# Kernel optimization log

Hardware: AMD Instinct MI355X
Metric: run time of the kernel (lower is better)

## Reference

```python
import jax, jax.numpy as jnp
import numpy as np

B, C, H, W = 16, 64, 224, 224
KS, STRIDE, PAD = 3, 2, 1
S = KS * KS           # patch_size = 9
G = C                 # group=1 -> inc//group = 64 independent ScannCore heads
P_SIDE = (H + 2 * PAD - KS) // STRIDE + 1   # 112
P = P_SIDE * P_SIDE                          # 12544 patches


def _unfold(x):
    """F.unfold(x, KS, 1, PAD, STRIDE) -> [B, C, S, Ph, Pw], (kh, kw) ordering."""
    xp = jnp.pad(x, ((0, 0), (0, 0), (PAD, PAD), (PAD, PAD)))
    end = 1 + STRIDE * (P_SIDE - 1)
    pats = [xp[:, :, kh:kh + end:STRIDE, kw:kw + end:STRIDE]
            for kh in range(KS) for kw in range(KS)]
    return jnp.stack(pats, axis=2)  # [B, C, S, Ph, Pw]


def setup_inputs() -> dict:
    key = jax.random.key(0)
    ks = jax.random.split(key, 10)
    x = jax.random.normal(ks[0], (B, C, H, W), dtype=jnp.float32)
    lim = 1.0 / np.sqrt(S)
    u = lambda k, shape: jax.random.uniform(k, shape, jnp.float32, -lim, lim)
    return {
        "x": x,
        "Wq": u(ks[1], (G, S, S)), "bq": u(ks[2], (G, S)),
        "Wk": u(ks[3], (G, S, S)), "bk": u(ks[4], (G, S)),
        "Wv": u(ks[5], (G, S, S)), "bv": u(ks[6], (G, S)),
        "Wo": u(ks[7], (G, 1, S)), "bo": u(ks[8], (G, 1)),
    }


def reference(x, Wq, bq, Wk, bk, Wv, bv, Wo, bo):
    # unfold -> [B, G, P, S] (group=1, so each channel is its own group)
    t = _unfold(x).reshape(B, G, S, P).transpose(0, 1, 3, 2)
    # per-group linear projections (torch Linear: y = x @ W.T + b)
    Q = jnp.einsum('bgps,gts->bgpt', t, Wq) + bq[None, :, None, :]
    K = jnp.einsum('bgps,gts->bgpt', t, Wk) + bk[None, :, None, :]
    V = jnp.einsum('bgps,gts->bgpt', t, Wv) + bv[None, :, None, :]
    # energy = K^T @ Q over the patch axis -> [B, G, S, S]
    energy = jnp.einsum('bgps,bgpt->bgst', K, Q)
    att = jax.nn.softmax(energy, axis=-1)
    # y = (att @ V^T)^T -> [B, G, P, S]
    y = jnp.einsum('bgst,bgpt->bgps', att, V)
    # out Linear(S -> 1), then fold back to [B, C, side, side]
    out = jnp.einsum('bgps,gos->bgpo', y, Wo) + bo[None, :, None, :]  # [B,G,P,1]
    return out[..., 0].reshape(B, G, P_SIDE, P_SIDE)
```

## Files before the change

kernel.cpp:

```cpp
#include <hip/hip_runtime.h>

#define HH 224
#define WW 224
#define PSD 112
#define NP 12544
#define NBG 1024
#define NCH 28
#define NTASK (112 * NCH)

#define MIDX(i, j) (9 * (i) - (i) * ((i)-1) / 2 + ((j) - (i)))
#define MAT(i, j) ((i) <= (j) ? sh[MIDX(i, j)] : sh[MIDX(j, i)])

__device__ __forceinline__ void load_row9(const float* __restrict__ row,
                                          int t, float* L) {
    const int cb = 8 * t;
    L[0] = (t == 0) ? 0.f : row[cb - 1];
    float4 a = *reinterpret_cast<const float4*>(row + cb);
    float4 b = *reinterpret_cast<const float4*>(row + cb + 4);
    L[1] = a.x; L[2] = a.y; L[3] = a.z; L[4] = a.w;
    L[5] = b.x; L[6] = b.y; L[7] = b.z; L[8] = b.w;
}

__global__ __launch_bounds__(256, 4) void scann_k(
    const float* __restrict__ x,
    const float* __restrict__ Wq, const float* __restrict__ bq,
    const float* __restrict__ Wk, const float* __restrict__ bk,
    const float* __restrict__ Wv, const float* __restrict__ bv,
    const float* __restrict__ Wo, const float* __restrict__ bo,
    float* __restrict__ out) {
    const int bg = blockIdx.x;
    const int g = bg & 63;
    const float* __restrict__ xp = x + (size_t)bg * (HH * WW);
    const int tid = threadIdx.x;

    __shared__ float red[4][56];
    __shared__ float sh[54];
    __shared__ float TT[81];
    __shared__ float Qm_s[9];
    __shared__ float wsh[81];
    __shared__ float cf[10];

    float acc[45];
    float sm[9];
#pragma unroll
    for (int k = 0; k < 45; ++k) acc[k] = 0.f;
#pragma unroll
    for (int i = 0; i < 9; ++i) sm[i] = 0.f;

    for (int task = tid; task < NTASK; task += 256) {
        const int ph = task / NCH;
        const int t = task - ph * NCH;
        const int r0 = 2 * ph - 1;
        float L[3][9];
#pragma unroll
        for (int kr = 0; kr < 3; ++kr) {
            const int r = r0 + kr;
            if (r < 0) {
#pragma unroll
                for (int j = 0; j < 9; ++j) L[kr][j] = 0.f;
            } else {
                load_row9(xp + r * WW, t, L[kr]);
            }
        }
#pragma unroll
        for (int u = 0; u < 4; ++u) {
            float v[9];
#pragma unroll
            for (int kh = 0; kh < 3; ++kh)
#pragma unroll
                for (int kw = 0; kw < 3; ++kw) v[3 * kh + kw] = L[kh][2 * u + kw];
            int k = 0;
#pragma unroll
            for (int i = 0; i < 9; ++i) {
                sm[i] += v[i];
#pragma unroll
                for (int j = i; j < 9; ++j) {
                    acc[k] += v[i] * v[j];
                    ++k;
                }
            }
        }
    }

    {
        const int lane = tid & 63;
        const int wv = tid >> 6;
#pragma unroll
        for (int k = 0; k < 45; ++k) {
            float v = acc[k];
#pragma unroll
            for (int off = 32; off; off >>= 1) v += __shfl_down(v, off, 64);
            if (lane == 0) red[wv][k] = v;
        }
#pragma unroll
        for (int i = 0; i < 9; ++i) {
            float v = sm[i];
#pragma unroll
            for (int off = 32; off; off >>= 1) v += __shfl_down(v, off, 64);
            if (lane == 0) red[wv][45 + i] = v;
        }
    }
    __syncthreads();
    if (tid < 54)
        sh[tid] = red[0][tid] + red[1][tid] + red[2][tid] + red[3][tid];
    __syncthreads();

    if (tid < 9) {
        const int t = tid;
        const float* wqt = Wq + g * 81 + t * 9;
        float w[9];
#pragma unroll
        for (int j = 0; j < 9; ++j) w[j] = wqt[j];
        float q = 0.f;
#pragma unroll
        for (int j = 0; j < 9; ++j) q += w[j] * sh[45 + j];
        Qm_s[t] = q;
#pragma unroll
        for (int i = 0; i < 9; ++i) {
            float s = 0.f;
#pragma unroll
            for (int j = 0; j < 9; ++j) s += MAT(i, j) * w[j];
            TT[i * 9 + t] = s;
        }
    }
    __syncthreads();
    if (tid < 9) {
        const int s = tid;
        const float* wks = Wk + g * 81 + s * 9;
        float w[9];
#pragma unroll
        for (int i = 0; i < 9; ++i) w[i] = wks[i];
        float Km = 0.f;
#pragma unroll
        for (int i = 0; i < 9; ++i) Km += w[i] * sh[45 + i];
        const float bks = bk[g * 9 + s];
        float e[9];
#pragma unroll
        for (int t = 0; t < 9; ++t) {
            const float bqt = bq[g * 9 + t];
            float sum = bks * Qm_s[t] + bqt * Km + 12544.f * bks * bqt;
#pragma unroll
            for (int i = 0; i < 9; ++i) sum += w[i] * TT[i * 9 + t];
            e[t] = sum;
        }
        float mx = e[0];
#pragma unroll
        for (int t = 1; t < 9; ++t) mx = fmaxf(mx, e[t]);
        float ex[9], se = 0.f;
#pragma unroll
        for (int t = 0; t < 9; ++t) {
            ex[t] = expf(e[t] - mx);
            se += ex[t];
        }
        const float wos = Wo[g * 9 + s] / se;
#pragma unroll
        for (int t = 0; t < 9; ++t) wsh[s * 9 + t] = wos * ex[t];
    }
    __syncthreads();
    if (tid < 9) {
        const int j = tid;
        float weff[9];
#pragma unroll
        for (int t = 0; t < 9; ++t) {
            float s = 0.f;
#pragma unroll
            for (int s2 = 0; s2 < 9; ++s2) s += wsh[s2 * 9 + t];
            weff[t] = s;
        }
        float cj = 0.f;
#pragma unroll
        for (int t = 0; t < 9; ++t) cj += weff[t] * Wv[g * 81 + t * 9 + j];
        cf[j] = cj;
        if (j == 0) {
            float d = bo[g];
#pragma unroll
            for (int t = 0; t < 9; ++t) d += weff[t] * bv[g * 9 + t];
            cf[9] = d;
        }
    }
    __syncthreads();

    float cc[9];
#pragma unroll
    for (int j = 0; j < 9; ++j) cc[j] = cf[j];
    const float dd = cf[9];
    float* __restrict__ op = out + (size_t)bg * NP;

    for (int task = tid; task < NTASK; task += 256) {
        const int ph = task / NCH;
        const int t = task - ph * NCH;
        const int r0 = 2 * ph - 1;
        float L[3][9];
#pragma unroll
        for (int kr = 0; kr < 3; ++kr) {
            const int r = r0 + kr;
            if (r < 0) {
#pragma unroll
                for (int j = 0; j < 9; ++j) L[kr][j] = 0.f;
            } else {
                load_row9(xp + r * WW, t, L[kr]);
            }
        }
        float o[4];
#pragma unroll
        for (int u = 0; u < 4; ++u) {
            float s = dd;
#pragma unroll
            for (int kh = 0; kh < 3; ++kh)
#pragma unroll
                for (int kw = 0; kw < 3; ++kw)
                    s += cc[3 * kh + kw] * L[kh][2 * u + kw];
            o[u] = s;
        }
        *reinterpret_cast<float4*>(op + ph * PSD + 4 * t) =
            make_float4(o[0], o[1], o[2], o[3]);
    }
}

extern "C" void kernel_launch(void* const* d_in, const int* in_sizes, int n_in,
                              void* d_out, int out_size, void* d_ws, size_t ws_size,
                              hipStream_t stream) {
    const float* x = (const float*)d_in[0];
    const float* Wq = (const float*)d_in[1];
    const float* bq = (const float*)d_in[2];
    const float* Wk = (const float*)d_in[3];
    const float* bk = (const float*)d_in[4];
    const float* Wv = (const float*)d_in[5];
    const float* bv = (const float*)d_in[6];
    const float* Wo = (const float*)d_in[7];
    const float* bo = (const float*)d_in[8];
    float* out = (float*)d_out;

    scann_k<<<NBG, 256, 0, stream>>>(x, Wq, bq, Wk, bk, Wv, bv, Wo, bo, out);
}
```

Before: 78.54 us.

## Stage input row bands in LDS before computing Gram and output passes

Both passes over the input image now copy 33-row bands cooperatively into shared memory with coalesced float4 loads. Each thread then reads its 3x9 window from LDS, so the strided 3-row overlap and the scalar left-halo global load no longer hit global memory. This adds about 30 KB of LDS per block and two barriers per band, which may limit occupancy and serialize loading with compute, since no double buffering is used.

```diff
diff --git a/kernel.cpp b/kernel.cpp
--- a/kernel.cpp
+++ b/kernel.cpp
@@ -6,33 +6,48 @@
 #define NP 12544
 #define NBG 1024
 #define NCH 28
-#define NTASK (112 * NCH)
-
-#define MIDX(i, j) (9 * (i) - (i) * ((i)-1) / 2 + ((j) - (i)))
-#define MAT(i, j) ((i) <= (j) ? sh[MIDX(i, j)] : sh[MIDX(j, i)])
-
-__device__ __forceinline__ void load_row9(const float* __restrict__ row,
-                                          int t, float* L) {
-    const int cb = 8 * t;
-    L[0] = (t == 0) ? 0.f : row[cb - 1];
-    float4 a = *reinterpret_cast<const float4*>(row + cb);
-    float4 b = *reinterpret_cast<const float4*>(row + cb + 4);
+#define PB 16
+#define NBAND 7
+#define BROWS 33
+#define LSTRIDE 228
+#define BQ (BROWS * WW / 4)
+
+__device__ __forceinline__ void stage_band(const float* __restrict__ xp,
+                                           float* __restrict__ band,
+                                           int b, int tid) {
+    const int r0 = 32 * b - 1;
+    for (int q = tid; q < BQ; q += 256) {
+        const int rl = q / 56;
+        const int c = (q - rl * 56) * 4;
+        const int r = r0 + rl;
+        float4 v = make_float4(0.f, 0.f, 0.f, 0.f);
+        if (r >= 0) v = *reinterpret_cast<const float4*>(xp + r * WW + c);
+        *reinterpret_cast<float4*>(band + rl * LSTRIDE + 4 + c) = v;
+    }
+    for (int i = tid; i < BROWS; i += 256) band[i * LSTRIDE + 3] = 0.f;
+}
+
+__device__ __forceinline__ void lds_row9(const float* __restrict__ rp, float* L) {
+    L[0] = rp[3];
+    float4 a = *reinterpret_cast<const float4*>(rp + 4);
+    float4 b = *reinterpret_cast<const float4*>(rp + 8);
     L[1] = a.x; L[2] = a.y; L[3] = a.z; L[4] = a.w;
     L[5] = b.x; L[6] = b.y; L[7] = b.z; L[8] = b.w;
 }
 
-__global__ __launch_bounds__(256, 4) void scann_k(
-    const float* __restrict__ x,
-    const float* __restrict__ Wq, const float* __restrict__ bq,
-    const float* __restrict__ Wk, const float* __restrict__ bk,
-    const float* __restrict__ Wv, const float* __restrict__ bv,
-    const float* __restrict__ Wo, const float* __restrict__ bo,
-    float* __restrict__ out) {
+__global__ void __launch_bounds__(256) __attribute__((amdgpu_waves_per_eu(4, 4)))
+scann_k(const float* __restrict__ x,
+        const float* __restrict__ Wq, const float* __restrict__ bq,
+        const float* __restrict__ Wk, const float* __restrict__ bk,
+        const float* __restrict__ Wv, const float* __restrict__ bv,
+        const float* __restrict__ Wo, const float* __restrict__ bo,
+        float* __restrict__ out) {
     const int bg = blockIdx.x;
     const int g = bg & 63;
     const float* __restrict__ xp = x + (size_t)bg * (HH * WW);
     const int tid = threadIdx.x;
 
+    __shared__ __align__(16) float band[BROWS * LSTRIDE];
     __shared__ float red[4][56];
     __shared__ float sh[54];
     __shared__ float TT[81];
@@ -47,39 +62,36 @@
 #pragma unroll
     for (int i = 0; i < 9; ++i) sm[i] = 0.f;
 
-    for (int task = tid; task < NTASK; task += 256) {
-        const int ph = task / NCH;
-        const int t = task - ph * NCH;
-        const int r0 = 2 * ph - 1;
-        float L[3][9];
-#pragma unroll
-        for (int kr = 0; kr < 3; ++kr) {
-            const int r = r0 + kr;
-            if (r < 0) {
-#pragma unroll
-                for (int j = 0; j < 9; ++j) L[kr][j] = 0.f;
-            } else {
-                load_row9(xp + r * WW, t, L[kr]);
-            }
-        }
-#pragma unroll
-        for (int u = 0; u < 4; ++u) {
-            float v[9];
-#pragma unroll
-            for (int kh = 0; kh < 3; ++kh)
-#pragma unroll
-                for (int kw = 0; kw < 3; ++kw) v[3 * kh + kw] = L[kh][2 * u + kw];
-            int k = 0;
-#pragma unroll
-            for (int i = 0; i < 9; ++i) {
-                sm[i] += v[i];
-#pragma unroll
-                for (int j = i; j < 9; ++j) {
-                    acc[k] += v[i] * v[j];
-                    ++k;
+    for (int b = 0; b < NBAND; ++b) {
+        stage_band(xp, band, b, tid);
+        __syncthreads();
+        for (int task = tid; task < PB * NCH; task += 256) {
+            const int phh = task / NCH;
+            const int t = task - phh * NCH;
+            const float* rowp = band + (2 * phh) * LSTRIDE + 8 * t;
+            float L[3][9];
+#pragma unroll
+            for (int kr = 0; kr < 3; ++kr) lds_row9(rowp + kr * LSTRIDE, L[kr]);
+#pragma unroll
+            for (int u = 0; u < 4; ++u) {
+                float v[9];
+#pragma unroll
+                for (int kh = 0; kh < 3; ++kh)
+#pragma unroll
+                    for (int kw = 0; kw < 3; ++kw) v[3 * kh + kw] = L[kh][2 * u + kw];
+                int k = 0;
+#pragma unroll
+                for (int i = 0; i < 9; ++i) {
+                    sm[i] += v[i];
+#pragma unroll
+                    for (int j = i; j < 9; ++j) {
+                        acc[k] += v[i] * v[j];
+                        ++k;
+                    }
                 }
             }
         }
+        __syncthreads();
     }
 
     {
@@ -105,6 +117,8 @@
         sh[tid] = red[0][tid] + red[1][tid] + red[2][tid] + red[3][tid];
     __syncthreads();
 
+#define MIDX(i, j) (9 * (i) - (i) * ((i)-1) / 2 + ((j) - (i)))
+#define MAT(i, j) ((i) <= (j) ? sh[MIDX(i, j)] : sh[MIDX(j, i)])
     if (tid < 9) {
         const int t = tid;
         const float* wqt = Wq + g * 81 + t * 9;
@@ -186,34 +200,32 @@
     const float dd = cf[9];
     float* __restrict__ op = out + (size_t)bg * NP;
 
-    for (int task = tid; task < NTASK; task += 256) {
-        const int ph = task / NCH;
-        const int t = task - ph * NCH;
-        const int r0 = 2 * ph - 1;
-        float L[3][9];
-#pragma unroll
-        for (int kr = 0; kr < 3; ++kr) {
-            const int r = r0 + kr;
-            if (r < 0) {
-#pragma unroll
-                for (int j = 0; j < 9; ++j) L[kr][j] = 0.f;
-            } else {
-                load_row9(xp + r * WW, t, L[kr]);
+    for (int b = 0; b < NBAND; ++b) {
+        stage_band(xp, band, b, tid);
+        __syncthreads();
+        for (int task = tid; task < PB * NCH; task += 256) {
+            const int phh = task / NCH;
+            const int t = task - phh * NCH;
+            const int ph = b * PB + phh;
+            const float* rowp = band + (2 * phh) * LSTRIDE + 8 * t;
+            float L[3][9];
+#pragma unroll
+            for (int kr = 0; kr < 3; ++kr) lds_row9(rowp + kr * LSTRIDE, L[kr]);
+            float o[4];
+#pragma unroll
+            for (int u = 0; u < 4; ++u) {
+                float s = dd;
+#pragma unroll
+                for (int kh = 0; kh < 3; ++kh)
+#pragma unroll
+                    for (int kw = 0; kw < 3; ++kw)
+                        s += cc[3 * kh + kw] * L[kh][2 * u + kw];
+                o[u] = s;
             }
-        }
-        float o[4];
-#pragma unroll
-        for (int u = 0; u < 4; ++u) {
-            float s = dd;
-#pragma unroll
-            for (int kh = 0; kh < 3; ++kh)
-#pragma unroll
-                for (int kw = 0; kw < 3; ++kw)
-                    s += cc[3 * kh + kw] * L[kh][2 * u + kw];
-            o[u] = s;
-        }
-        *reinterpret_cast<float4*>(op + ph * PSD + 4 * t) =
-            make_float4(o[0], o[1], o[2], o[3]);
+            *reinterpret_cast<float4*>(op + ph * PSD + 4 * t) =
+                make_float4(o[0], o[1], o[2], o[3]);
+        }
+        __syncthreads();
     }
 }
 
```

After: 126.2 us. 1.61x slower.

## Split Gram-matrix entries across waves instead of splitting patches across threads

Applied to the files above, without the earlier changes.

In the statistics pass, each of the four waves now walks every patch of the block but accumulates only its own subset of the 45 Gram entries and 9 column sums. Before, each thread handled a quarter of the patches and accumulated all 54 values. The change cuts per-thread accumulator registers and removes the shared-memory cross-wave reduction plus one barrier. In exchange, every wave re-reads the whole input plane, so global/cache load traffic in the first pass grows about fourfold, and the wave workloads are slightly unbalanced.

```diff
diff --git a/kernel.cpp b/kernel.cpp
--- a/kernel.cpp
+++ b/kernel.cpp
@@ -8,8 +8,10 @@
 #define NCH 28
 #define NTASK (112 * NCH)
 
-#define MIDX(i, j) (9 * (i) - (i) * ((i)-1) / 2 + ((j) - (i)))
-#define MAT(i, j) ((i) <= (j) ? sh[MIDX(i, j)] : sh[MIDX(j, i)])
+constexpr int PI[45] = {0,0,0,0,0,0,0,0,0, 1,1,1,1,1,1,1,1, 2,2,2,2,2,2,2,
+                        3,3,3,3,3,3, 4,4,4,4,4, 5,5,5,5, 6,6,6, 7,7, 8};
+constexpr int PJ[45] = {0,1,2,3,4,5,6,7,8, 1,2,3,4,5,6,7,8, 2,3,4,5,6,7,8,
+                        3,4,5,6,7,8, 4,5,6,7,8, 5,6,7,8, 6,7,8, 7,8, 8};
 
 __device__ __forceinline__ void load_row9(const float* __restrict__ row,
                                           int t, float* L) {
@@ -19,6 +21,65 @@
     float4 b = *reinterpret_cast<const float4*>(row + cb + 4);
     L[1] = a.x; L[2] = a.y; L[3] = a.z; L[4] = a.w;
     L[5] = b.x; L[6] = b.y; L[7] = b.z; L[8] = b.w;
+}
+
+template <int K0, int K1, int S0, int S1>
+__device__ __forceinline__ void gram_wave(const float* __restrict__ xp,
+                                          int lane, float* __restrict__ sh) {
+    constexpr int NK = K1 - K0;
+    constexpr int NS = S1 - S0;
+    float acc[NK];
+    float sm[NS];
+#pragma unroll
+    for (int m = 0; m < NK; ++m) acc[m] = 0.f;
+#pragma unroll
+    for (int m = 0; m < NS; ++m) sm[m] = 0.f;
+
+    for (int q = 0; q < NTASK / 64; ++q) {
+        const int task = q * 64 + lane;
+        const int ph = task / NCH;
+        const int t = task - ph * NCH;
+        const int r0 = 2 * ph - 1;
+        float L[3][9];
+#pragma unroll
+        for (int kr = 0; kr < 3; ++kr) {
+            const int r = r0 + kr;
+            if (r < 0) {
+#pragma unroll
+                for (int j = 0; j < 9; ++j) L[kr][j] = 0.f;
+            } else {
+                load_row9(xp + r * WW, t, L[kr]);
+            }
+        }
+#pragma unroll
+        for (int u = 0; u < 4; ++u) {
+#pragma unroll
+            for (int k = K0; k < K1; ++k) {
+                constexpr int z = 0;
+                (void)z;
+                const int i = PI[k], j = PJ[k];
+                acc[k - K0] += L[i / 3][2 * u + i % 3] * L[j / 3][2 * u + j % 3];
+            }
+#pragma unroll
+            for (int i2 = S0; i2 < S1; ++i2)
+                sm[i2 - S0] += L[i2 / 3][2 * u + i2 % 3];
+        }
+    }
+
+#pragma unroll
+    for (int m = 0; m < NK; ++m) {
+        float v = acc[m];
+#pragma unroll
+        for (int off = 32; off; off >>= 1) v += __shfl_down(v, off, 64);
+        if (lane == 0) sh[K0 + m] = v;
+    }
+#pragma unroll
+    for (int m = 0; m < NS; ++m) {
+        float v = sm[m];
+#pragma unroll
+        for (int off = 32; off; off >>= 1) v += __shfl_down(v, off, 64);
+        if (lane == 0) sh[45 + S0 + m] = v;
+    }
 }
 
 __global__ __launch_bounds__(256, 4) void scann_k(
@@ -32,79 +93,23 @@
     const int g = bg & 63;
     const float* __restrict__ xp = x + (size_t)bg * (HH * WW);
     const int tid = threadIdx.x;
-
-    __shared__ float red[4][56];
+    const int wv = tid >> 6;
+    const int lane = tid & 63;
+
     __shared__ float sh[54];
     __shared__ float TT[81];
     __shared__ float Qm_s[9];
     __shared__ float wsh[81];
     __shared__ float cf[10];
 
-    float acc[45];
-    float sm[9];
-#pragma unroll
-    for (int k = 0; k < 45; ++k) acc[k] = 0.f;
-#pragma unroll
-    for (int i = 0; i < 9; ++i) sm[i] = 0.f;
-
-    for (int task = tid; task < NTASK; task += 256) {
-        const int ph = task / NCH;
-        const int t = task - ph * NCH;
-        const int r0 = 2 * ph - 1;
-        float L[3][9];
-#pragma unroll
-        for (int kr = 0; kr < 3; ++kr) {
-            const int r = r0 + kr;
-            if (r < 0) {
-#pragma unroll
-                for (int j = 0; j < 9; ++j) L[kr][j] = 0.f;
-            } else {
-                load_row9(xp + r * WW, t, L[kr]);
-            }
-        }
-#pragma unroll
-        for (int u = 0; u < 4; ++u) {
-            float v[9];
-#pragma unroll
-            for (int kh = 0; kh < 3; ++kh)
-#pragma unroll
-                for (int kw = 0; kw < 3; ++kw) v[3 * kh + kw] = L[kh][2 * u + kw];
-            int k = 0;
-#pragma unroll
-            for (int i = 0; i < 9; ++i) {
-                sm[i] += v[i];
-#pragma unroll
-                for (int j = i; j < 9; ++j) {
-                    acc[k] += v[i] * v[j];
-                    ++k;
-                }
-            }
-        }
-    }
-
-    {
-        const int lane = tid & 63;
-        const int wv = tid >> 6;
-#pragma unroll
-        for (int k = 0; k < 45; ++k) {
-            float v = acc[k];
-#pragma unroll
-            for (int off = 32; off; off >>= 1) v += __shfl_down(v, off, 64);
-            if (lane == 0) red[wv][k] = v;
-        }
-#pragma unroll
-        for (int i = 0; i < 9; ++i) {
-            float v = sm[i];
-#pragma unroll
-            for (int off = 32; off; off >>= 1) v += __shfl_down(v, off, 64);
-            if (lane == 0) red[wv][45 + i] = v;
-        }
-    }
-    __syncthreads();
-    if (tid < 54)
-        sh[tid] = red[0][tid] + red[1][tid] + red[2][tid] + red[3][tid];
-    __syncthreads();
-
+    if (wv == 0)      gram_wave<0, 11, 0, 2>(xp, lane, sh);
+    else if (wv == 1) gram_wave<11, 22, 2, 4>(xp, lane, sh);
+    else if (wv == 2) gram_wave<22, 33, 4, 6>(xp, lane, sh);
+    else              gram_wave<33, 45, 6, 9>(xp, lane, sh);
+    __syncthreads();
+
+#define MIDX(i, j) (9 * (i) - (i) * ((i)-1) / 2 + ((j) - (i)))
+#define MAT(i, j) ((i) <= (j) ? sh[MIDX(i, j)] : sh[MIDX(j, i)])
     if (tid < 9) {
         const int t = tid;
         const float* wqt = Wq + g * 81 + t * 9;
```

Measured after the change: 136.0 us. +73.1%, slower.
